# Optimization experiments

Hardware: AMD Instinct MI355X
Metric: run time of the kernel (lower is better)

## Reference

```python
import jax, jax.numpy as jnp
import numpy as np
import math

IN_FEATURES = 4096
OUT_FEATURES = 4096
NUM_COMPONENTS = 256
TWO_PI = 2.0 * math.pi


def setup_inputs() -> dict:
    key = jax.random.key(0)
    k1, k2, k3, k4 = jax.random.split(key, 4)
    x = jax.random.normal(k1, (4096, IN_FEATURES), dtype=jnp.float32)
    mus = jax.random.uniform(k2, (NUM_COMPONENTS, 2), dtype=jnp.float32)
    log_vars = -3.0 - jax.random.uniform(k3, (NUM_COMPONENTS, 2), dtype=jnp.float32)
    weights = jax.random.uniform(k4, (NUM_COMPONENTS,), dtype=jnp.float32) / NUM_COMPONENTS
    return {"x": x, "mus": mus, "log_vars": log_vars, "weights": weights}


def reference(x, mus, log_vars, weights):
    in_features = x.shape[1]
    x_in_idx = jnp.linspace(0.0, 1.0, in_features, dtype=jnp.float32)    # [I]
    x_out_idx = jnp.linspace(0.0, 1.0, OUT_FEATURES, dtype=jnp.float32)  # [O]
    vars_ = jnp.exp(log_vars)  # [M, 2]

    # Input-side Gaussian basis, fused with 1/sqrt(2*pi*var) and component weight: [I, M]
    d_in = (x_in_idx[:, None] - mus[None, :, 0]) ** 2
    G_in = jnp.exp(-d_in / (2.0 * vars_[None, :, 0])) / jnp.sqrt(TWO_PI * vars_[None, :, 0]) * weights[None, :]
    C = x @ G_in  # [B, M]

    # Output-side Gaussian pdf (Normal(mu1, sigma1).log_prob(x_out).exp()): [M, O]
    d_out = (x_out_idx[None, :] - mus[:, 1:2]) ** 2
    G_out = jnp.exp(-d_out / (2.0 * vars_[:, 1:2])) / jnp.sqrt(TWO_PI * vars_[:, 1:2])

    x_out = (C @ G_out) / (in_features * jnp.sum(weights))  # [B, O]
    return x_out
```

## Files before the change

kernel.cpp:

```cpp
#include <hip/hip_runtime.h>
#include <hip/hip_bf16.h>
#include <math.h>

#define IN_FEAT 4096
#define OUT_FEAT 4096
#define NCOMP 256
#define BATCH 4096
#define TWO_PI_F 6.28318530717958647692f

typedef __attribute__((ext_vector_type(8))) short short8;
typedef __attribute__((ext_vector_type(8))) __bf16 bf16x8;
typedef __attribute__((ext_vector_type(4))) float f32x4;

__device__ __forceinline__ ushort f2b(float f) {
  union { float f; unsigned u; } v; v.f = f;
  unsigned r = (v.u + 0x7fffu + ((v.u >> 16) & 1u)) >> 16;
  return (ushort)r;
}

__device__ __forceinline__ float b2f(short s) {
  union { unsigned u; float f; } v; v.u = ((unsigned)(ushort)s) << 16;
  return v.f;
}

__device__ __forceinline__ bf16x8 ld_frag(const void* p) {
  short8 s = *(const short8*)p;
  return __builtin_bit_cast(bf16x8, s);
}

__device__ __forceinline__ short8 cvt8(float4 a, float4 b) {
  short8 h;
  h[0] = (short)f2b(a.x); h[1] = (short)f2b(a.y);
  h[2] = (short)f2b(a.z); h[3] = (short)f2b(a.w);
  h[4] = (short)f2b(b.x); h[5] = (short)f2b(b.y);
  h[6] = (short)f2b(b.z); h[7] = (short)f2b(b.w);
  return h;
}

__device__ __forceinline__ void gload_lds16(const ushort* g, ushort* l) {
  __builtin_amdgcn_global_load_lds(
      (const __attribute__((address_space(1))) void*)g,
      (__attribute__((address_space(3))) void*)l, 16, 0, 0);
}

__global__ __launch_bounds__(256) void prep_kernel(
    const float* __restrict__ mus, const float* __restrict__ lvs,
    const float* __restrict__ w,
    ushort* __restrict__ Gt, ushort* __restrict__ GoT) {
  int idx = blockIdx.x * 256 + threadIdx.x;
  if (idx < NCOMP * IN_FEAT) {
    int m = idx >> 12, i = idx & (IN_FEAT - 1);
    float v = expf(lvs[2 * m]);
    float d = (float)i * (1.0f / (IN_FEAT - 1)) - mus[2 * m];
    float g = expf(-d * d * (0.5f / v)) * rsqrtf(TWO_PI_F * v) * w[m];
    Gt[idx] = f2b(g);
  } else {
    idx -= NCOMP * IN_FEAT;
    int o = idx >> 8, m = idx & (NCOMP - 1);
    float v = expf(lvs[2 * m + 1]);
    float d = (float)o * (1.0f / (OUT_FEAT - 1)) - mus[2 * m + 1];
    float g = expf(-d * d * (0.5f / v)) * rsqrtf(TWO_PI_F * v);
    GoT[idx] = f2b(g);
  }
}

template<int NS>
__global__ __launch_bounds__(256, 4) void gemm1_kernel(
    const float* __restrict__ x, const ushort* __restrict__ Gt,
    ushort* __restrict__ Cpart) {
  constexpr int KR = IN_FEAT / NS;
  constexpr int NT = KR / 32;
  __shared__ __align__(16) ushort lds[2 * 10240];
  const int tid = threadIdx.x, wid = tid >> 6, lane = tid & 63;
  const int m0 = blockIdx.x * 64;
  const int kb0 = blockIdx.y * KR;

  f32x4 acc[16] = {};

  const int brow = lane >> 2;
  const int bswz = (((lane & 3) ^ ((lane >> 3) & 3)) << 3);
  const int fswz = ((lane >> 4) << 4) ^ ((((lane & 15) >> 1) & 3) << 4);

  const int arow = tid >> 2, aslot = tid & 3;
  const float* asrc = &x[(size_t)(m0 + arow) * IN_FEAT + kb0 + aslot * 8];
  const int abyte = arow * 64 + ((aslot << 4) ^ (((arow >> 1) & 3) << 4));

  #define STAGE_B(buf, kb)                                                   \
    _Pragma("unroll")                                                        \
    for (int q = 0; q < 4; ++q) {                                            \
      int nb = wid * 4 + q;                                                  \
      gload_lds16(&Gt[(size_t)(nb * 16 + brow) * IN_FEAT + (kb) + bswz],     \
                  &lds[(buf) * 10240 + nb * 512]);                           \
    }

  STAGE_B(0, kb0)
  {
    float4 a0 = *(const float4*)asrc;
    float4 a1 = *(const float4*)(asrc + 4);
    *(short8*)((char*)lds + 16384 + abyte) = cvt8(a0, a1);
  }
  __syncthreads();

  for (int t = 0; t < NT; ++t) {
    float4 px0, px1;
    if (t + 1 < NT) {
      STAGE_B((t + 1) & 1, kb0 + (t + 1) * 32)
      px0 = *(const float4*)(asrc + (t + 1) * 32);
      px1 = *(const float4*)(asrc + (t + 1) * 32 + 4);
    }
    const char* base = (const char*)lds + (t & 1) * 20480;
    bf16x8 af = ld_frag(base + 16384 + (wid * 16 + (lane & 15)) * 64 + fswz);
    #pragma unroll
    for (int nj = 0; nj < 16; ++nj) {
      bf16x8 bf = ld_frag(base + (nj * 16 + (lane & 15)) * 64 + fswz);
      acc[nj] = __builtin_amdgcn_mfma_f32_16x16x32_bf16(af, bf, acc[nj], 0, 0, 0);
    }
    if (t + 1 < NT)
      *(short8*)((char*)lds + ((t + 1) & 1) * 20480 + 16384 + abyte) =
          cvt8(px0, px1);
    __syncthreads();
  }
  #undef STAGE_B

  ushort* Cp = Cpart + (size_t)blockIdx.y * ((size_t)BATCH * NCOMP);
  #pragma unroll
  for (int nj = 0; nj < 16; ++nj)
    #pragma unroll
    for (int r = 0; r < 4; ++r) {
      int row = m0 + wid * 16 + (lane >> 4) * 4 + r;
      int col = nj * 16 + (lane & 15);
      Cp[(size_t)row * NCOMP + col] = f2b(acc[nj][r]);
    }
}

template<int NS>
__global__ __launch_bounds__(256) void reduce_kernel(ushort* __restrict__ Cp) {
  size_t i = ((size_t)blockIdx.x * 256 + threadIdx.x) * 8;
  float s[8] = {};
  #pragma unroll
  for (int p = 0; p < NS; ++p) {
    short8 v = *(const short8*)&Cp[(size_t)p * BATCH * NCOMP + i];
    #pragma unroll
    for (int e = 0; e < 8; ++e) s[e] += b2f(v[e]);
  }
  short8 h;
  #pragma unroll
  for (int e = 0; e < 8; ++e) h[e] = (short)f2b(s[e]);
  *(short8*)&Cp[i] = h;
}

__global__ __launch_bounds__(256, 4) void gemm2_kernel(
    const ushort* __restrict__ Cb, const ushort* __restrict__ GoT,
    const float* __restrict__ w, float* __restrict__ out) {
  __shared__ __align__(16) ushort lds[2 * 8192];
  const int tid = threadIdx.x, wid = tid >> 6, lane = tid & 63;
  const int m0 = blockIdx.y * 128, n0 = blockIdx.x * 128;
  const int wr = (wid >> 1) * 64, wc = (wid & 1) * 64;

  float4 wv = *(const float4*)&w[lane * 4];
  float s = wv.x + wv.y + wv.z + wv.w;
  #pragma unroll
  for (int off = 32; off > 0; off >>= 1) s += __shfl_xor(s, off);
  const float scale = 1.0f / ((float)IN_FEAT * s);

  const int brow = lane >> 2;
  const int bswz = (((lane & 3) ^ ((lane >> 3) & 3)) << 3);
  const int fswz = ((lane >> 4) << 4) ^ ((((lane & 15) >> 1) & 3) << 4);

  f32x4 acc[4][4] = {};

  #define STAGE2(buf, k0)                                                    \
    _Pragma("unroll")                                                        \
    for (int q = 0; q < 2; ++q) {                                            \
      int c = wid * 2 + q;                                                   \
      int row = c * 16 + brow;                                               \
      gload_lds16(&Cb[(size_t)(m0 + row) * NCOMP + (k0) + bswz],             \
                  &lds[(buf) * 8192 + c * 512]);                             \
      gload_lds16(&GoT[(size_t)(n0 + row) * NCOMP + (k0) + bswz],            \
                  &lds[(buf) * 8192 + 4096 + c * 512]);                      \
    }

  STAGE2(0, 0)
  __syncthreads();

  for (int t = 0; t < 8; ++t) {
    if (t < 7) STAGE2((t + 1) & 1, (t + 1) * 32)
    const char* base = (const char*)lds + (t & 1) * 16384;
    bf16x8 af[4], bf[4];
    #pragma unroll
    for (int i = 0; i < 4; ++i)
      af[i] = ld_frag(base + (wr + i * 16 + (lane & 15)) * 64 + fswz);
    #pragma unroll
    for (int j = 0; j < 4; ++j)
      bf[j] = ld_frag(base + 8192 + (wc + j * 16 + (lane & 15)) * 64 + fswz);
    #pragma unroll
    for (int i = 0; i < 4; ++i)
      #pragma unroll
      for (int j = 0; j < 4; ++j)
        acc[i][j] = __builtin_amdgcn_mfma_f32_16x16x32_bf16(af[i], bf[j], acc[i][j], 0, 0, 0);
    __syncthreads();
  }
  #undef STAGE2

  #pragma unroll
  for (int i = 0; i < 4; ++i)
    #pragma unroll
    for (int r = 0; r < 4; ++r) {
      int row = m0 + wr + i * 16 + (lane >> 4) * 4 + r;
      #pragma unroll
      for (int j = 0; j < 4; ++j)
        out[(size_t)row * OUT_FEAT + n0 + wc + j * 16 + (lane & 15)] =
            acc[i][j][r] * scale;
    }
}

extern "C" void kernel_launch(void* const* d_in, const int* in_sizes, int n_in,
                              void* d_out, int out_size, void* d_ws, size_t ws_size,
                              hipStream_t stream) {
  const float* x   = (const float*)d_in[0];
  const float* mus = (const float*)d_in[1];
  const float* lvs = (const float*)d_in[2];
  const float* w   = (const float*)d_in[3];
  float* out = (float*)d_out;

  ushort* Gt  = (ushort*)d_ws;
  ushort* GoT = Gt  + (size_t)NCOMP * IN_FEAT;
  ushort* Cpart = GoT + (size_t)OUT_FEAT * NCOMP;

  const size_t MiB = 1024 * 1024;
  int nsplit = 16;
  while (nsplit > 1 && ws_size < 4 * MiB + (size_t)nsplit * 2 * MiB) nsplit >>= 1;

  prep_kernel<<<(NCOMP * IN_FEAT + OUT_FEAT * NCOMP) / 256, 256, 0, stream>>>(
      mus, lvs, w, Gt, GoT);

  dim3 g1(BATCH / 64, nsplit);
  switch (nsplit) {
    case 16: gemm1_kernel<16><<<g1, 256, 0, stream>>>(x, Gt, Cpart);
             reduce_kernel<16><<<BATCH * NCOMP / 8 / 256, 256, 0, stream>>>(Cpart);
             break;
    case 8:  gemm1_kernel<8><<<g1, 256, 0, stream>>>(x, Gt, Cpart);
             reduce_kernel<8><<<BATCH * NCOMP / 8 / 256, 256, 0, stream>>>(Cpart);
             break;
    case 4:  gemm1_kernel<4><<<g1, 256, 0, stream>>>(x, Gt, Cpart);
             reduce_kernel<4><<<BATCH * NCOMP / 8 / 256, 256, 0, stream>>>(Cpart);
             break;
    case 2:  gemm1_kernel<2><<<g1, 256, 0, stream>>>(x, Gt, Cpart);
             reduce_kernel<2><<<BATCH * NCOMP / 8 / 256, 256, 0, stream>>>(Cpart);
             break;
    default: gemm1_kernel<1><<<g1, 256, 0, stream>>>(x, Gt, Cpart);
             break;
  }

  gemm2_kernel<<<dim3(OUT_FEAT / 128, BATCH / 128), 256, 0, stream>>>(
      Cpart, GoT, w, out);
}
```

Measured before the change: 60.77 us.

## Switch both GEMMs from 16x16x32 to 32x32x16 bf16 MFMA tiles

```diff
diff --git a/kernel.cpp b/kernel.cpp
--- a/kernel.cpp
+++ b/kernel.cpp
@@ -11,6 +11,7 @@
 typedef __attribute__((ext_vector_type(8))) short short8;
 typedef __attribute__((ext_vector_type(8))) __bf16 bf16x8;
 typedef __attribute__((ext_vector_type(4))) float f32x4;
+typedef __attribute__((ext_vector_type(16))) float f32x16;
 
 __device__ __forceinline__ ushort f2b(float f) {
   union { float f; unsigned u; } v; v.f = f;
@@ -74,16 +75,16 @@
   const int tid = threadIdx.x, wid = tid >> 6, lane = tid & 63;
   const int m0 = blockIdx.x * 64;
   const int kb0 = blockIdx.y * KR;
-
-  f32x4 acc[16] = {};
+  const int r32 = lane & 31, h = lane >> 5;
+
+  f32x16 acc[2][2] = {};
 
   const int brow = lane >> 2;
   const int bswz = (((lane & 3) ^ ((lane >> 3) & 3)) << 3);
-  const int fswz = ((lane >> 4) << 4) ^ ((((lane & 15) >> 1) & 3) << 4);
-
   const int arow = tid >> 2, aslot = tid & 3;
   const float* asrc = &x[(size_t)(m0 + arow) * IN_FEAT + kb0 + aslot * 8];
   const int abyte = arow * 64 + ((aslot << 4) ^ (((arow >> 1) & 3) << 4));
+  const int sw0 = (h << 4) ^ (((r32 >> 1) & 3) << 4);
 
   #define STAGE_B(buf, kb)                                                   \
     _Pragma("unroll")                                                        \
@@ -93,10 +94,10 @@
                   &lds[(buf) * 10240 + nb * 512]);                           \
     }
 
-  STAGE_B(0, kb0)
   {
     float4 a0 = *(const float4*)asrc;
     float4 a1 = *(const float4*)(asrc + 4);
+    STAGE_B(0, kb0)
     *(short8*)((char*)lds + 16384 + abyte) = cvt8(a0, a1);
   }
   __syncthreads();
@@ -104,16 +105,23 @@
   for (int t = 0; t < NT; ++t) {
     float4 px0, px1;
     if (t + 1 < NT) {
-      STAGE_B((t + 1) & 1, kb0 + (t + 1) * 32)
       px0 = *(const float4*)(asrc + (t + 1) * 32);
       px1 = *(const float4*)(asrc + (t + 1) * 32 + 4);
+      STAGE_B((t + 1) & 1, kb0 + (t + 1) * 32)
     }
     const char* base = (const char*)lds + (t & 1) * 20480;
-    bf16x8 af = ld_frag(base + 16384 + (wid * 16 + (lane & 15)) * 64 + fswz);
-    #pragma unroll
-    for (int nj = 0; nj < 16; ++nj) {
-      bf16x8 bf = ld_frag(base + (nj * 16 + (lane & 15)) * 64 + fswz);
-      acc[nj] = __builtin_amdgcn_mfma_f32_16x16x32_bf16(af, bf, acc[nj], 0, 0, 0);
+    const char* Ab = base + 16384;
+    #pragma unroll
+    for (int s = 0; s < 2; ++s) {
+      const int off = sw0 ^ (s << 5);
+      bf16x8 a0 = ld_frag(Ab + r32 * 64 + off);
+      bf16x8 a1 = ld_frag(Ab + (32 + r32) * 64 + off);
+      bf16x8 b0 = ld_frag(base + (wid * 64 + r32) * 64 + off);
+      bf16x8 b1 = ld_frag(base + (wid * 64 + 32 + r32) * 64 + off);
+      acc[0][0] = __builtin_amdgcn_mfma_f32_32x32x16_bf16(a0, b0, acc[0][0], 0, 0, 0);
+      acc[0][1] = __builtin_amdgcn_mfma_f32_32x32x16_bf16(a0, b1, acc[0][1], 0, 0, 0);
+      acc[1][0] = __builtin_amdgcn_mfma_f32_32x32x16_bf16(a1, b0, acc[1][0], 0, 0, 0);
+      acc[1][1] = __builtin_amdgcn_mfma_f32_32x32x16_bf16(a1, b1, acc[1][1], 0, 0, 0);
     }
     if (t + 1 < NT)
       *(short8*)((char*)lds + ((t + 1) & 1) * 20480 + 16384 + abyte) =
@@ -124,13 +132,15 @@
 
   ushort* Cp = Cpart + (size_t)blockIdx.y * ((size_t)BATCH * NCOMP);
   #pragma unroll
-  for (int nj = 0; nj < 16; ++nj)
-    #pragma unroll
-    for (int r = 0; r < 4; ++r) {
-      int row = m0 + wid * 16 + (lane >> 4) * 4 + r;
-      int col = nj * 16 + (lane & 15);
-      Cp[(size_t)row * NCOMP + col] = f2b(acc[nj][r]);
-    }
+  for (int mi = 0; mi < 2; ++mi)
+    #pragma unroll
+    for (int nj = 0; nj < 2; ++nj)
+      #pragma unroll
+      for (int g = 0; g < 16; ++g) {
+        int row = m0 + mi * 32 + (g & 3) + 8 * (g >> 2) + 4 * h;
+        int col = wid * 64 + nj * 32 + r32;
+        Cp[(size_t)row * NCOMP + col] = f2b(acc[mi][nj][g]);
+      }
 }
 
 template<int NS>
@@ -143,10 +153,10 @@
     #pragma unroll
     for (int e = 0; e < 8; ++e) s[e] += b2f(v[e]);
   }
-  short8 h;
-  #pragma unroll
-  for (int e = 0; e < 8; ++e) h[e] = (short)f2b(s[e]);
-  *(short8*)&Cp[i] = h;
+  short8 hh;
+  #pragma unroll
+  for (int e = 0; e < 8; ++e) hh[e] = (short)f2b(s[e]);
+  *(short8*)&Cp[i] = hh;
 }
 
 __global__ __launch_bounds__(256, 4) void gemm2_kernel(
@@ -156,6 +166,7 @@
   const int tid = threadIdx.x, wid = tid >> 6, lane = tid & 63;
   const int m0 = blockIdx.y * 128, n0 = blockIdx.x * 128;
   const int wr = (wid >> 1) * 64, wc = (wid & 1) * 64;
+  const int r32 = lane & 31, h = lane >> 5;
 
   float4 wv = *(const float4*)&w[lane * 4];
   float s = wv.x + wv.y + wv.z + wv.w;
@@ -165,9 +176,9 @@
 
   const int brow = lane >> 2;
   const int bswz = (((lane & 3) ^ ((lane >> 3) & 3)) << 3);
-  const int fswz = ((lane >> 4) << 4) ^ ((((lane & 15) >> 1) & 3) << 4);
-
-  f32x4 acc[4][4] = {};
+  const int sw0 = (h << 4) ^ (((r32 >> 1) & 3) << 4);
+
+  f32x16 acc[2][2] = {};
 
   #define STAGE2(buf, k0)                                                    \
     _Pragma("unroll")                                                        \
@@ -186,32 +197,33 @@
   for (int t = 0; t < 8; ++t) {
     if (t < 7) STAGE2((t + 1) & 1, (t + 1) * 32)
     const char* base = (const char*)lds + (t & 1) * 16384;
-    bf16x8 af[4], bf[4];
-    #pragma unroll
-    for (int i = 0; i < 4; ++i)
-      af[i] = ld_frag(base + (wr + i * 16 + (lane & 15)) * 64 + fswz);
-    #pragma unroll
-    for (int j = 0; j < 4; ++j)
-      bf[j] = ld_frag(base + 8192 + (wc + j * 16 + (lane & 15)) * 64 + fswz);
-    #pragma unroll
-    for (int i = 0; i < 4; ++i)
+    const char* Bb = base + 8192;
+    #pragma unroll
+    for (int s2 = 0; s2 < 2; ++s2) {
+      const int off = sw0 ^ (s2 << 5);
+      bf16x8 a0 = ld_frag(base + (wr + r32) * 64 + off);
+      bf16x8 a1 = ld_frag(base + (wr + 32 + r32) * 64 + off);
+      bf16x8 b0 = ld_frag(Bb + (wc + r32) * 64 + off);
+      bf16x8 b1 = ld_frag(Bb + (wc + 32 + r32) * 64 + off);
+      acc[0][0] = __builtin_amdgcn_mfma_f32_32x32x16_bf16(a0, b0, acc[0][0], 0, 0, 0);
+      acc[0][1] = __builtin_amdgcn_mfma_f32_32x32x16_bf16(a0, b1, acc[0][1], 0, 0, 0);
+      acc[1][0] = __builtin_amdgcn_mfma_f32_32x32x16_bf16(a1, b0, acc[1][0], 0, 0, 0);
+      acc[1][1] = __builtin_amdgcn_mfma_f32_32x32x16_bf16(a1, b1, acc[1][1], 0, 0, 0);
+    }
+    __syncthreads();
+  }
+  #undef STAGE2
+
+  #pragma unroll
+  for (int mi = 0; mi < 2; ++mi)
+    #pragma unroll
+    for (int nj = 0; nj < 2; ++nj)
       #pragma unroll
-      for (int j = 0; j < 4; ++j)
-        acc[i][j] = __builtin_amdgcn_mfma_f32_16x16x32_bf16(af[i], bf[j], acc[i][j], 0, 0, 0);
-    __syncthreads();
-  }
-  #undef STAGE2
-
-  #pragma unroll
-  for (int i = 0; i < 4; ++i)
-    #pragma unroll
-    for (int r = 0; r < 4; ++r) {
-      int row = m0 + wr + i * 16 + (lane >> 4) * 4 + r;
-      #pragma unroll
-      for (int j = 0; j < 4; ++j)
-        out[(size_t)row * OUT_FEAT + n0 + wc + j * 16 + (lane & 15)] =
-            acc[i][j][r] * scale;
-    }
+      for (int g = 0; g < 16; ++g) {
+        int row = m0 + wr + mi * 32 + (g & 3) + 8 * (g >> 2) + 4 * h;
+        int col = n0 + wc + nj * 32 + r32;
+        out[(size_t)row * OUT_FEAT + col] = acc[mi][nj][g] * scale;
+      }
 }
 
 extern "C" void kernel_launch(void* const* d_in, const int* in_sizes, int n_in,
```

Result: slower. 62.14 us (+2.3%).
